# Optimization experiments

Measured on AMD Instinct MI355X. Metric: run time of the kernel, lower is better.

Reference implementation:

```python
import jax, jax.numpy as jnp
import numpy as np

N_NODES = 100000
N_EDGES = 3200000
N_GRAPHS = 64
F_IN = 64
NUM_CLASSES = 10
CHROM = 21


def _glorot(key, shape):
    fan_in, fan_out = shape
    lim = (6.0 / (fan_in + fan_out)) ** 0.5
    return jax.random.uniform(key, shape, jnp.float32, -lim, lim)


def setup_inputs() -> dict:
    key = jax.random.key(0)
    ks = jax.random.split(key, 16)
    x = jax.random.normal(ks[0], (N_NODES, F_IN), jnp.float32)
    edge_index = jax.random.randint(ks[1], (2, N_EDGES), 0, N_NODES, jnp.int32)
    batch = jnp.sort(jax.random.randint(ks[2], (N_NODES,), 0, N_GRAPHS, jnp.int32))
    return {
        "x": x,
        "edge_index": edge_index,
        "batch": batch,
        # SAGEConv1: 64 -> 16
        "W1l": _glorot(ks[3], (F_IN, 16)), "b1": jnp.zeros((16,), jnp.float32),
        "W1r": _glorot(ks[4], (F_IN, 16)),
        # SAGEConv2: 16 -> 32
        "W2l": _glorot(ks[5], (16, 32)), "b2": jnp.zeros((32,), jnp.float32),
        "W2r": _glorot(ks[6], (16, 32)),
        # SAGEConv3: 32 -> 21
        "W3l": _glorot(ks[7], (32, CHROM)), "b3": jnp.zeros((CHROM,), jnp.float32),
        "W3r": _glorot(ks[8], (32, CHROM)),
        # classifier: 32 -> num_classes
        "Wc": _glorot(ks[9], (32, NUM_CLASSES)), "bc": jnp.zeros((NUM_CLASSES,), jnp.float32),
    }


def _sage_conv(x, src, dst, Wl, b, Wr):
    # mean aggregation of source features at target nodes (PyG SAGEConv default)
    agg = jax.ops.segment_sum(x[src], dst, num_segments=N_NODES)
    cnt = jax.ops.segment_sum(jnp.ones((src.shape[0],), x.dtype), dst, num_segments=N_NODES)
    mean = agg / jnp.maximum(cnt, 1.0)[:, None]
    return mean @ Wl + b + x @ Wr


def reference(x, edge_index, batch, W1l, b1, W1r, W2l, b2, W2r, W3l, b3, W3r, Wc, bc):
    src, dst = edge_index[0], edge_index[1]
    h = jax.nn.relu(_sage_conv(x, src, dst, W1l, b1, W1r))
    h2 = _sage_conv(h, src, dst, W2l, b2, W2r)          # pooled pre-relu
    color = _sage_conv(jax.nn.relu(h2), src, dst, W3l, b3, W3r)
    # global_mean_pool over graphs
    gsum = jax.ops.segment_sum(h2, batch, num_segments=N_GRAPHS)
    gcnt = jax.ops.segment_sum(jnp.ones((h2.shape[0],), h2.dtype), batch, num_segments=N_GRAPHS)
    pooled = gsum / jnp.maximum(gcnt, 1.0)[:, None]
    # dropout p=0.3 is identity in eval mode
    classif = pooled @ Wc + bc
    return classif, color
```

## Files before the change

### kernel.cpp

```cpp
#include <hip/hip_runtime.h>
#include <hip/hip_fp16.h>
#include <cstdint>
#include <cstddef>

#define N_NODES  100000
#define N_EDGES  3200000
#define N_GRAPHS 64

#define BQBITS   9
#define BQ       512
#define NBUCK    196
#define TILE     4096
#define NBLK     782
#define POOL_SLICES 8
#define PADB     4608

typedef float vf2 __attribute__((ext_vector_type(2)));


__global__ void kp1_hist(const int* __restrict__ dst, int* __restrict__ gh, int ne) {
    __shared__ int h[NBUCK];
    for (int i = threadIdx.x; i < NBUCK; i += 256) h[i] = 0;
    __syncthreads();
    int base = blockIdx.x * TILE;
    for (int i = threadIdx.x; i < TILE; i += 256) {
        int e = base + i;
        if (e < ne) atomicAdd(&h[dst[e] >> BQBITS], 1);
    }
    __syncthreads();
    for (int i = threadIdx.x; i < NBUCK; i += 256) gh[i * NBLK + blockIdx.x] = h[i];
}

__global__ void kp1_scanA(int* __restrict__ gh, int* __restrict__ btotal) {
    int q = blockIdx.x;
    __shared__ int ts[256];
    int v[4];
    int tsum = 0;
#pragma unroll
    for (int u = 0; u < 4; ++u) {
        int idx = threadIdx.x * 4 + u;
        v[u] = (idx < NBLK) ? gh[q * NBLK + idx] : 0;
        tsum += v[u];
    }
    ts[threadIdx.x] = tsum;
    __syncthreads();
    for (int off = 1; off < 256; off <<= 1) {
        int t = (threadIdx.x >= off) ? ts[threadIdx.x - off] : 0;
        __syncthreads();
        ts[threadIdx.x] += t;
        __syncthreads();
    }
    int run = ts[threadIdx.x] - tsum;
#pragma unroll
    for (int u = 0; u < 4; ++u) {
        int idx = threadIdx.x * 4 + u;
        if (idx < NBLK) gh[q * NBLK + idx] = run;
        run += v[u];
    }
    if (threadIdx.x == 255) btotal[q] = ts[255];
}

__global__ void kp1_scanB(const int* __restrict__ btotal, int* __restrict__ bstart) {
    __shared__ int s[256];
    int v = (threadIdx.x < NBUCK) ? btotal[threadIdx.x] : 0;
    s[threadIdx.x] = v;
    __syncthreads();
    for (int off = 1; off < 256; off <<= 1) {
        int t = (threadIdx.x >= off) ? s[threadIdx.x - off] : 0;
        __syncthreads();
        s[threadIdx.x] += t;
        __syncthreads();
    }
    if (threadIdx.x < NBUCK) bstart[threadIdx.x] = s[threadIdx.x] - v;
    if (threadIdx.x == 0) bstart[NBUCK] = N_EDGES;
}

__global__ __launch_bounds__(256) void kp1_scatter(
        const int* __restrict__ src, const int* __restrict__ dst,
        const int* __restrict__ gh, const int* __restrict__ bstart,
        unsigned* __restrict__ tmp, int ne) {
    __shared__ unsigned sed[TILE];
    __shared__ int lcnt[NBUCK];
    __shared__ int lofs[NBUCK + 1];
    __shared__ int fill[NBUCK];
    __shared__ int delta[NBUCK];
    __shared__ int ts[256];
    for (int i = threadIdx.x; i < NBUCK; i += 256) { lcnt[i] = 0; fill[i] = 0; }
    __syncthreads();
    int base = blockIdx.x * TILE;
    int nh = ne - base; if (nh > TILE) nh = TILE;
    int myq[16]; unsigned myw[16];
#pragma unroll
    for (int u = 0; u < 16; ++u) {
        int i = u * 256 + threadIdx.x;
        myq[u] = -1;
        if (i < nh) {
            int d = dst[base + i], s = src[base + i];
            int q = d >> BQBITS;
            myq[u] = q;
            myw[u] = ((unsigned)(d & (BQ - 1)) << 17) | (unsigned)s;
            atomicAdd(&lcnt[q], 1);
        }
    }
    __syncthreads();
    int v = (threadIdx.x < NBUCK) ? lcnt[threadIdx.x] : 0;
    ts[threadIdx.x] = v;
    __syncthreads();
    for (int off = 1; off < 256; off <<= 1) {
        int t = (threadIdx.x >= off) ? ts[threadIdx.x - off] : 0;
        __syncthreads();
        ts[threadIdx.x] += t;
        __syncthreads();
    }
    if (threadIdx.x < NBUCK) {
        int start = ts[threadIdx.x] - v;
        lofs[threadIdx.x] = start;
        delta[threadIdx.x] = bstart[threadIdx.x] + gh[threadIdx.x * NBLK + blockIdx.x] - start;
    }
    if (threadIdx.x == NBUCK - 1) lofs[NBUCK] = ts[threadIdx.x];
    __syncthreads();
#pragma unroll
    for (int u = 0; u < 16; ++u) {
        if (myq[u] >= 0) {
            int r = atomicAdd(&fill[myq[u]], 1);
            sed[lofs[myq[u]] + r] = myw[u];
        }
    }
    __syncthreads();
    for (int p = threadIdx.x; p < nh; p += 256) {
        int lo = 0, hi = NBUCK;
        while (hi - lo > 1) { int mid = (lo + hi) >> 1; if (lofs[mid] <= p) lo = mid; else hi = mid; }
        tmp[p + delta[lo]] = sed[p];
    }
}

__global__ void kp2(const unsigned* __restrict__ tmp, const int* __restrict__ bstart,
                    int* __restrict__ rs, int* __restrict__ deg, int* __restrict__ perm) {
    int q = blockIdx.x;
    int beg = bstart[q], end = bstart[q + 1];
    int m = end - beg;
    int pbase = ((beg + 7) & ~7) + q * PADB;
    __shared__ int cnt[BQ];
    __shared__ int lofs[BQ];
    __shared__ int fill[BQ];
    if (threadIdx.x < BQ) { cnt[threadIdx.x] = 0; fill[threadIdx.x] = 0; }
    __syncthreads();
    for (int p = threadIdx.x; p < m; p += 1024)
        atomicAdd(&cnt[tmp[beg + p] >> 17], 1);
    __syncthreads();
    int pc = 0;
    if (threadIdx.x < BQ) { pc = (cnt[threadIdx.x] + 7) & ~7; lofs[threadIdx.x] = pc; }
    __syncthreads();
    for (int off = 1; off < BQ; off <<= 1) {
        int t = 0;
        if (threadIdx.x < BQ && threadIdx.x >= off) t = lofs[threadIdx.x - off];
        __syncthreads();
        if (threadIdx.x < BQ) lofs[threadIdx.x] += t;
        __syncthreads();
    }
    if (threadIdx.x < BQ) {
        int node = q * BQ + threadIdx.x;
        if (node < N_NODES) {
            int st = lofs[threadIdx.x] - pc;
            rs[node] = pbase + st;
            deg[node] = cnt[threadIdx.x];
            for (int i = cnt[threadIdx.x]; i < pc; ++i)
                perm[pbase + st + i] = N_NODES;
        }
    }
    __syncthreads();
    for (int p = threadIdx.x; p < m; p += 1024) {
        unsigned w = tmp[beg + p];
        int dl = w >> 17;
        int s = w & 0x1FFFF;
        int r = atomicAdd(&fill[dl], 1);
        int st = lofs[dl] - ((cnt[dl] + 7) & ~7);
        perm[pbase + st + r] = s;
    }
}


__device__ __forceinline__ void accq(uint2 v, float* a) {
    vf2 f0 = __builtin_amdgcn_cvt_pk_f32_fp8((int)v.x, false);
    vf2 f1 = __builtin_amdgcn_cvt_pk_f32_fp8((int)v.x, true);
    vf2 f2 = __builtin_amdgcn_cvt_pk_f32_fp8((int)v.y, false);
    vf2 f3 = __builtin_amdgcn_cvt_pk_f32_fp8((int)v.y, true);
    a[0] += f0.x; a[1] += f0.y; a[2] += f1.x; a[3] += f1.y;
    a[4] += f2.x; a[5] += f2.y; a[6] += f3.x; a[7] += f3.y;
}

__device__ __forceinline__ uint2 pack8_fp8(const float* a) {
    int lo = __builtin_amdgcn_cvt_pk_fp8_f32(a[0], a[1], 0, false);
    lo     = __builtin_amdgcn_cvt_pk_fp8_f32(a[2], a[3], lo, true);
    int hi = __builtin_amdgcn_cvt_pk_fp8_f32(a[4], a[5], 0, false);
    hi     = __builtin_amdgcn_cvt_pk_fp8_f32(a[6], a[7], hi, true);
    uint2 o; o.x = (unsigned)lo; o.y = (unsigned)hi; return o;
}


__global__ void k_zero(uint2* __restrict__ y1qz, uint2* __restrict__ hqz,
                       unsigned char* __restrict__ y3qz, float* __restrict__ gsum) {
    int t = threadIdx.x;
    if (t < 2) { y1qz[t] = make_uint2(0, 0); hqz[t] = make_uint2(0, 0); }
    if (t < 24) y3qz[t] = 0;
    for (int i = t; i < N_GRAPHS * 32; i += 256) gsum[i] = 0.f;
}


__global__ void k_t1(const float* __restrict__ x, const float* __restrict__ W1l,
                     const float* __restrict__ W1r, const float* __restrict__ b1,
                     uint2* __restrict__ y1q, float* __restrict__ s1, int n) {
    __shared__ float wl[64 * 16], wr[64 * 16], bb[16];
    for (int i = threadIdx.x; i < 64 * 16; i += blockDim.x) { wl[i] = W1l[i]; wr[i] = W1r[i]; }
    if (threadIdx.x < 16) bb[threadIdx.x] = b1[threadIdx.x];
    __syncthreads();
    int node = blockIdx.x * blockDim.x + threadIdx.x;
    if (node >= n) return;
    const float4* xr = reinterpret_cast<const float4*>(x + (size_t)node * 64);
    float accl[16], accr[16];
#pragma unroll
    for (int j = 0; j < 16; ++j) { accl[j] = 0.f; accr[j] = 0.f; }
#pragma unroll
    for (int q = 0; q < 16; ++q) {
        float4 v = xr[q];
        float xs[4] = {v.x, v.y, v.z, v.w};
#pragma unroll
        for (int u = 0; u < 4; ++u) {
            int k = q * 4 + u;
            float xv = xs[u];
#pragma unroll
            for (int j = 0; j < 16; ++j) {
                accl[j] += xv * wl[k * 16 + j];
                accr[j] += xv * wr[k * 16 + j];
            }
        }
    }
    y1q[(size_t)node * 2 + 0] = pack8_fp8(accl);
    y1q[(size_t)node * 2 + 1] = pack8_fp8(accl + 8);
    float4* s4 = reinterpret_cast<float4*>(s1 + (size_t)node * 16);
#pragma unroll
    for (int q = 0; q < 4; ++q)
        s4[q] = make_float4(accr[q*4+0] + bb[q*4+0], accr[q*4+1] + bb[q*4+1],
                            accr[q*4+2] + bb[q*4+2], accr[q*4+3] + bb[q*4+3]);
}

__global__ void k_t2(const float* __restrict__ mean2, const __half* __restrict__ h,
                     const float* __restrict__ W2l, const float* __restrict__ W2r,
                     const float* __restrict__ b2, float* __restrict__ h2, int n) {
    __shared__ float wl[16 * 32], wr[16 * 32], bb[32];
    for (int i = threadIdx.x; i < 16 * 32; i += blockDim.x) { wl[i] = W2l[i]; wr[i] = W2r[i]; }
    if (threadIdx.x < 32) bb[threadIdx.x] = b2[threadIdx.x];
    __syncthreads();
    int node = blockIdx.x * blockDim.x + threadIdx.x;
    if (node >= n) return;
    float m[16], hh[16];
    const float4* m4 = reinterpret_cast<const float4*>(mean2 + (size_t)node * 16);
#pragma unroll
    for (int q = 0; q < 4; ++q) {
        float4 a = m4[q];
        m[q*4+0]=a.x; m[q*4+1]=a.y; m[q*4+2]=a.z; m[q*4+3]=a.w;
    }
    alignas(16) __half hv[16];
    const uint4* hp = reinterpret_cast<const uint4*>(h + (size_t)node * 16);
    uint4* hvp = reinterpret_cast<uint4*>(hv);
    hvp[0] = hp[0]; hvp[1] = hp[1];
#pragma unroll
    for (int k = 0; k < 16; ++k) hh[k] = __half2float(hv[k]);
    float acc[32];
#pragma unroll
    for (int j = 0; j < 32; ++j) acc[j] = bb[j];
#pragma unroll
    for (int k = 0; k < 16; ++k) {
#pragma unroll
        for (int j = 0; j < 32; ++j)
            acc[j] += m[k] * wl[k * 32 + j] + hh[k] * wr[k * 32 + j];
    }
    float4* o4 = reinterpret_cast<float4*>(h2 + (size_t)node * 32);
#pragma unroll
    for (int q = 0; q < 8; ++q)
        o4[q] = make_float4(acc[q*4+0], acc[q*4+1], acc[q*4+2], acc[q*4+3]);
}

__global__ void k_t3(const float* __restrict__ h2, const float* __restrict__ W3l,
                     const float* __restrict__ W3r, const float* __restrict__ b3,
                     unsigned char* __restrict__ y3q, float* __restrict__ s3, int n) {
    __shared__ float wl[32 * 21], wr[32 * 21], bb[21];
    for (int i = threadIdx.x; i < 32 * 21; i += blockDim.x) { wl[i] = W3l[i]; wr[i] = W3r[i]; }
    if (threadIdx.x < 21) bb[threadIdx.x] = b3[threadIdx.x];
    __syncthreads();
    int node = blockIdx.x * blockDim.x + threadIdx.x;
    if (node >= n) return;
    float z[32];
    const float4* h4 = reinterpret_cast<const float4*>(h2 + (size_t)node * 32);
#pragma unroll
    for (int q = 0; q < 8; ++q) {
        float4 v = h4[q];
        z[q*4+0] = fmaxf(v.x, 0.f); z[q*4+1] = fmaxf(v.y, 0.f);
        z[q*4+2] = fmaxf(v.z, 0.f); z[q*4+3] = fmaxf(v.w, 0.f);
    }
    float a[24], c[21];
#pragma unroll
    for (int j = 0; j < 21; ++j) { a[j] = 0.f; c[j] = bb[j]; }
    a[21] = 0.f; a[22] = 0.f; a[23] = 0.f;
#pragma unroll
    for (int k = 0; k < 32; ++k) {
#pragma unroll
        for (int j = 0; j < 21; ++j) {
            a[j] += z[k] * wl[k * 21 + j];
            c[j] += z[k] * wr[k * 21 + j];
        }
    }
    uint2* yp = reinterpret_cast<uint2*>(y3q + (size_t)node * 24);
    yp[0] = pack8_fp8(a);
    yp[1] = pack8_fp8(a + 8);
    yp[2] = pack8_fp8(a + 16);
    float* so = s3 + (size_t)node * 24;
#pragma unroll
    for (int j = 0; j < 21; ++j) so[j] = c[j];
    so[21] = 0.f; so[22] = 0.f; so[23] = 0.f;
}


__global__ void k_agg_l1(const uint2* __restrict__ yq, const int* __restrict__ rs,
                         const int* __restrict__ deg, const int* __restrict__ perm,
                         const float* __restrict__ s1, __half* __restrict__ h,
                         uint2* __restrict__ hq, int n_nodes) {
    int t = blockIdx.x * blockDim.x + threadIdx.x;
    int node = t >> 1;
    int f = t & 1;
    if (node >= n_nodes) return;
    int beg = rs[node];
    int d = deg[node];
    int pend = beg + ((d + 7) & ~7);
    float a[8];
#pragma unroll
    for (int j = 0; j < 8; ++j) a[j] = 0.f;
    for (int e = beg; e < pend; e += 8) {
        const int4* pp = reinterpret_cast<const int4*>(perm + e);
        int4 p0 = pp[0];
        int4 p1 = pp[1];
        uint2 v0 = yq[(size_t)p0.x * 2 + f];
        uint2 v1 = yq[(size_t)p0.y * 2 + f];
        uint2 v2 = yq[(size_t)p0.z * 2 + f];
        uint2 v3 = yq[(size_t)p0.w * 2 + f];
        uint2 v4 = yq[(size_t)p1.x * 2 + f];
        uint2 v5 = yq[(size_t)p1.y * 2 + f];
        uint2 v6 = yq[(size_t)p1.z * 2 + f];
        uint2 v7 = yq[(size_t)p1.w * 2 + f];
        accq(v0, a); accq(v1, a); accq(v2, a); accq(v3, a);
        accq(v4, a); accq(v5, a); accq(v6, a); accq(v7, a);
    }
    float inv = 1.0f / fmaxf((float)d, 1.0f);
    const float4* sp = reinterpret_cast<const float4*>(s1 + (size_t)node * 16 + f * 8);
    float4 s0 = sp[0], s1v = sp[1];
    a[0] = fmaxf(a[0] * inv + s0.x, 0.f);
    a[1] = fmaxf(a[1] * inv + s0.y, 0.f);
    a[2] = fmaxf(a[2] * inv + s0.z, 0.f);
    a[3] = fmaxf(a[3] * inv + s0.w, 0.f);
    a[4] = fmaxf(a[4] * inv + s1v.x, 0.f);
    a[5] = fmaxf(a[5] * inv + s1v.y, 0.f);
    a[6] = fmaxf(a[6] * inv + s1v.z, 0.f);
    a[7] = fmaxf(a[7] * inv + s1v.w, 0.f);
    __half2 p0h = __floats2half2_rn(a[0], a[1]);
    __half2 p1h = __floats2half2_rn(a[2], a[3]);
    __half2 p2h = __floats2half2_rn(a[4], a[5]);
    __half2 p3h = __floats2half2_rn(a[6], a[7]);
    uint4 o;
    o.x = *reinterpret_cast<unsigned*>(&p0h);
    o.y = *reinterpret_cast<unsigned*>(&p1h);
    o.z = *reinterpret_cast<unsigned*>(&p2h);
    o.w = *reinterpret_cast<unsigned*>(&p3h);
    reinterpret_cast<uint4*>(h)[(size_t)node * 2 + f] = o;
    hq[(size_t)node * 2 + f] = pack8_fp8(a);
}

__global__ void k_agg_l2(const uint2* __restrict__ hq, const int* __restrict__ rs,
                         const int* __restrict__ deg, const int* __restrict__ perm,
                         float* __restrict__ mean2, int n_nodes) {
    int t = blockIdx.x * blockDim.x + threadIdx.x;
    int node = t >> 1;
    int f = t & 1;
    if (node >= n_nodes) return;
    int beg = rs[node];
    int d = deg[node];
    int pend = beg + ((d + 7) & ~7);
    float a[8];
#pragma unroll
    for (int j = 0; j < 8; ++j) a[j] = 0.f;
    for (int e = beg; e < pend; e += 8) {
        const int4* pp = reinterpret_cast<const int4*>(perm + e);
        int4 p0 = pp[0];
        int4 p1 = pp[1];
        uint2 v0 = hq[(size_t)p0.x * 2 + f];
        uint2 v1 = hq[(size_t)p0.y * 2 + f];
        uint2 v2 = hq[(size_t)p0.z * 2 + f];
        uint2 v3 = hq[(size_t)p0.w * 2 + f];
        uint2 v4 = hq[(size_t)p1.x * 2 + f];
        uint2 v5 = hq[(size_t)p1.y * 2 + f];
        uint2 v6 = hq[(size_t)p1.z * 2 + f];
        uint2 v7 = hq[(size_t)p1.w * 2 + f];
        accq(v0, a); accq(v1, a); accq(v2, a); accq(v3, a);
        accq(v4, a); accq(v5, a); accq(v6, a); accq(v7, a);
    }
    float inv = 1.0f / fmaxf((float)d, 1.0f);
    float4* op = reinterpret_cast<float4*>(mean2 + (size_t)node * 16 + f * 8);
    op[0] = make_float4(a[0] * inv, a[1] * inv, a[2] * inv, a[3] * inv);
    op[1] = make_float4(a[4] * inv, a[5] * inv, a[6] * inv, a[7] * inv);
}

__global__ void k_agg_l3(const unsigned char* __restrict__ y3q, const int* __restrict__ rs,
                         const int* __restrict__ deg, const int* __restrict__ perm,
                         const float* __restrict__ self24, float* __restrict__ outp,
                         int n_nodes) {
    int t = blockIdx.x * blockDim.x + threadIdx.x;
    int node = t / 3;
    int f = t - node * 3;
    if (node >= n_nodes) return;
    const uint2* yq = reinterpret_cast<const uint2*>(y3q);
    int beg = rs[node];
    int d = deg[node];
    int pend = beg + ((d + 7) & ~7);
    float a[8];
#pragma unroll
    for (int j = 0; j < 8; ++j) a[j] = 0.f;
    for (int e = beg; e < pend; e += 8) {
        const int4* pp = reinterpret_cast<const int4*>(perm + e);
        int4 p0 = pp[0];
        int4 p1 = pp[1];
        uint2 v0 = yq[(size_t)p0.x * 3 + f];
        uint2 v1 = yq[(size_t)p0.y * 3 + f];
        uint2 v2 = yq[(size_t)p0.z * 3 + f];
        uint2 v3 = yq[(size_t)p0.w * 3 + f];
        uint2 v4 = yq[(size_t)p1.x * 3 + f];
        uint2 v5 = yq[(size_t)p1.y * 3 + f];
        uint2 v6 = yq[(size_t)p1.z * 3 + f];
        uint2 v7 = yq[(size_t)p1.w * 3 + f];
        accq(v0, a); accq(v1, a); accq(v2, a); accq(v3, a);
        accq(v4, a); accq(v5, a); accq(v6, a); accq(v7, a);
    }
    float inv = 1.0f / fmaxf((float)d, 1.0f);
    int c0 = f * 8;
    const float4* sp = reinterpret_cast<const float4*>(self24 + (size_t)node * 24 + c0);
    float4 s0 = sp[0], s1 = sp[1];
    float r[8];
    r[0] = a[0] * inv + s0.x; r[1] = a[1] * inv + s0.y;
    r[2] = a[2] * inv + s0.z; r[3] = a[3] * inv + s0.w;
    r[4] = a[4] * inv + s1.x; r[5] = a[5] * inv + s1.y;
    r[6] = a[6] * inv + s1.z; r[7] = a[7] * inv + s1.w;
    float* op = outp + (size_t)node * 21;
    int nlim = 21 - c0;
#pragma unroll
    for (int j = 0; j < 8; ++j)
        if (j < nlim) op[c0 + j] = r[j];
}


__device__ __forceinline__ int lowerb(const int* a, int n, int key) {
    int lo = 0, hi = n;
    while (lo < hi) { int mid = (lo + hi) >> 1; if (a[mid] < key) lo = mid + 1; else hi = mid; }
    return lo;
}

__global__ void k_pool(const float* __restrict__ h2, const int* __restrict__ batch,
                       float* __restrict__ gsum, float* __restrict__ gcnt, int n) {
    int g = blockIdx.x / POOL_SLICES;
    int slice = blockIdx.x - g * POOL_SLICES;
    __shared__ int sbeg, send;
    if (threadIdx.x == 0) { sbeg = lowerb(batch, n, g); send = lowerb(batch, n, g + 1); }
    __syncthreads();
    int beg = sbeg, end = send;
    int f = threadIdx.x & 31;
    int r = threadIdx.x >> 5;
    float acc = 0.f;
    for (int i = beg + slice * 8 + r; i < end; i += POOL_SLICES * 8)
        acc += h2[(size_t)i * 32 + f];
    __shared__ float red[256];
    red[threadIdx.x] = acc;
    __syncthreads();
    if (r == 0) {
        float s = 0.f;
#pragma unroll
        for (int q = 0; q < 8; ++q) s += red[q * 32 + f];
        atomicAdd(&gsum[g * 32 + f], s);
    }
    if (slice == 0 && threadIdx.x == 0) gcnt[g] = (float)(end - beg);
}

__global__ void k_cls(const float* __restrict__ gsum, const float* __restrict__ gcnt,
                      const float* __restrict__ Wc, const float* __restrict__ bc,
                      float* __restrict__ outp) {
    int t = threadIdx.x;
    if (t >= N_GRAPHS * 10) return;
    int g = t / 10, c = t - g * 10;
    float cv = fmaxf(gcnt[g], 1.f);
    float acc = bc[c];
#pragma unroll
    for (int k = 0; k < 32; ++k) acc += (gsum[g * 32 + k] / cv) * Wc[k * 10 + c];
    outp[g * 10 + c] = acc;
}


extern "C" void kernel_launch(void* const* d_in, const int* in_sizes, int n_in,
                              void* d_out, int out_size, void* d_ws, size_t ws_size,
                              hipStream_t stream) {
    const float* x    = (const float*)d_in[0];
    const int*   ei   = (const int*)d_in[1];
    const int*   batch= (const int*)d_in[2];
    const float* W1l  = (const float*)d_in[3];
    const float* b1   = (const float*)d_in[4];
    const float* W1r  = (const float*)d_in[5];
    const float* W2l  = (const float*)d_in[6];
    const float* b2   = (const float*)d_in[7];
    const float* W2r  = (const float*)d_in[8];
    const float* W3l  = (const float*)d_in[9];
    const float* b3   = (const float*)d_in[10];
    const float* W3r  = (const float*)d_in[11];
    const float* Wc   = (const float*)d_in[12];
    const float* bc   = (const float*)d_in[13];
    float* out = (float*)d_out;

    char* ws = (char*)d_ws;
    size_t off = 0;
    auto alloc = [&](size_t bytes) { size_t o = off; off += (bytes + 255) & ~(size_t)255; return o; };

    int*    rs    = (int*)(ws + alloc((size_t)N_NODES * 4));
    int*    deg   = (int*)(ws + alloc((size_t)N_NODES * 4));
    int*    perm  = (int*)(ws + alloc((size_t)(N_EDGES + (size_t)NBUCK * PADB + 64) * 4));
    int*    gh    = (int*)(ws + alloc((size_t)NBUCK * NBLK * 4));
    int*    btotal= (int*)(ws + alloc(256 * 4));
    int*    bstart= (int*)(ws + alloc(260 * 4));
    uint2*  y1q   = (uint2*)(ws + alloc((size_t)(N_NODES + 1) * 16));
    float*  s1    = (float*)(ws + alloc((size_t)N_NODES * 16 * 4));
    __half* h     = (__half*)(ws + alloc((size_t)N_NODES * 16 * 2));
    uint2*  hq    = (uint2*)(ws + alloc((size_t)(N_NODES + 1) * 16));
    float*  mean2 = (float*)(ws + alloc((size_t)N_NODES * 16 * 4));
    float*  h2    = (float*)(ws + alloc((size_t)N_NODES * 32 * 4));
    unsigned char* y3q = (unsigned char*)(ws + alloc((size_t)(N_NODES + 1) * 24));
    float*  s3    = (float*)(ws + alloc((size_t)N_NODES * 24 * 4));
    float*  gsum  = (float*)(ws + alloc((size_t)N_GRAPHS * 32 * 4));
    float*  gcnt  = (float*)(ws + alloc((size_t)N_GRAPHS * 4));

    unsigned* tmp = (unsigned*)h2;

    const int* src = ei;
    const int* dst = ei + N_EDGES;

    int nb  = (N_NODES + 255) / 256;
    int g2  = (N_NODES * 2 + 255) / 256;
    int g3  = (N_NODES * 3 + 255) / 256;

    k_zero<<<1, 256, 0, stream>>>(y1q + (size_t)N_NODES * 2, hq + (size_t)N_NODES * 2,
                                  y3q + (size_t)N_NODES * 24, gsum);

    kp1_hist   <<<NBLK, 256, 0, stream>>>(dst, gh, N_EDGES);
    kp1_scanA  <<<NBUCK, 256, 0, stream>>>(gh, btotal);
    kp1_scanB  <<<1, 256, 0, stream>>>(btotal, bstart);
    kp1_scatter<<<NBLK, 256, 0, stream>>>(src, dst, gh, bstart, tmp, N_EDGES);
    kp2        <<<NBUCK, 1024, 0, stream>>>(tmp, bstart, rs, deg, perm);

    k_t1<<<nb, 256, 0, stream>>>(x, W1l, W1r, b1, y1q, s1, N_NODES);
    k_agg_l1<<<g2, 256, 0, stream>>>(y1q, rs, deg, perm, s1, h, hq, N_NODES);

    k_agg_l2<<<g2, 256, 0, stream>>>(hq, rs, deg, perm, mean2, N_NODES);
    k_t2<<<nb, 256, 0, stream>>>(mean2, h, W2l, W2r, b2, h2, N_NODES);

    k_t3<<<nb, 256, 0, stream>>>(h2, W3l, W3r, b3, y3q, s3, N_NODES);
    k_agg_l3<<<g3, 256, 0, stream>>>(y3q, rs, deg, perm, s3, out + N_GRAPHS * 10, N_NODES);

    k_pool<<<N_GRAPHS * POOL_SLICES, 256, 0, stream>>>(h2, batch, gsum, gcnt, N_NODES);
    k_cls<<<1, 640, 0, stream>>>(gsum, gcnt, Wc, bc, out);
}
```

Before: 214.9 us.

## Fuse layer-2/3 transforms with graph pooling and drop zero kernel

Merges the k_t2 and k_t3 node transforms into one kernel, so h2 stays in registers and is no longer written to and re-read from global memory. Each block reduces its h2 rows per graph in shared memory and atomically adds them into gsum, which replaces the separate pooling kernel. The zeroing work moves into scanB, and graph counts are now computed by binary search inside k_cls, together removing three launches. The cost is a large shared buffer that may reduce occupancy, a serial 256-row reduction done by a single wavefront per block, and tmp now needing its own workspace allocation.

Measured after the change: 203.0 us. 5.5% less time.

```diff
diff --git a/kernel.cpp b/kernel.cpp
--- a/kernel.cpp
+++ b/kernel.cpp
@@ -12,7 +12,6 @@
 #define NBUCK    196
 #define TILE     4096
 #define NBLK     782
-#define POOL_SLICES 8
 #define PADB     4608
 
 typedef float vf2 __attribute__((ext_vector_type(2)));
@@ -60,7 +59,9 @@
     if (threadIdx.x == 255) btotal[q] = ts[255];
 }
 
-__global__ void kp1_scanB(const int* __restrict__ btotal, int* __restrict__ bstart) {
+__global__ void kp1_scanB(const int* __restrict__ btotal, int* __restrict__ bstart,
+                          uint2* __restrict__ y1qz, uint2* __restrict__ hqz,
+                          unsigned char* __restrict__ y3qz, float* __restrict__ gsum) {
     __shared__ int s[256];
     int v = (threadIdx.x < NBUCK) ? btotal[threadIdx.x] : 0;
     s[threadIdx.x] = v;
@@ -73,6 +74,10 @@
     }
     if (threadIdx.x < NBUCK) bstart[threadIdx.x] = s[threadIdx.x] - v;
     if (threadIdx.x == 0) bstart[NBUCK] = N_EDGES;
+    int t = threadIdx.x;
+    if (t < 2) { y1qz[t] = make_uint2(0, 0); hqz[t] = make_uint2(0, 0); }
+    if (t < 24) y3qz[t] = 0;
+    for (int i = t; i < N_GRAPHS * 32; i += 256) gsum[i] = 0.f;
 }
 
 __global__ __launch_bounds__(256) void kp1_scatter(
@@ -198,15 +203,6 @@
 }
 
 
-__global__ void k_zero(uint2* __restrict__ y1qz, uint2* __restrict__ hqz,
-                       unsigned char* __restrict__ y3qz, float* __restrict__ gsum) {
-    int t = threadIdx.x;
-    if (t < 2) { y1qz[t] = make_uint2(0, 0); hqz[t] = make_uint2(0, 0); }
-    if (t < 24) y3qz[t] = 0;
-    for (int i = t; i < N_GRAPHS * 32; i += 256) gsum[i] = 0.f;
-}
-
-
 __global__ void k_t1(const float* __restrict__ x, const float* __restrict__ W1l,
                      const float* __restrict__ W1r, const float* __restrict__ b1,
                      uint2* __restrict__ y1q, float* __restrict__ s1, int n) {
@@ -244,80 +240,94 @@
                             accr[q*4+2] + bb[q*4+2], accr[q*4+3] + bb[q*4+3]);
 }
 
-__global__ void k_t2(const float* __restrict__ mean2, const __half* __restrict__ h,
-                     const float* __restrict__ W2l, const float* __restrict__ W2r,
-                     const float* __restrict__ b2, float* __restrict__ h2, int n) {
-    __shared__ float wl[16 * 32], wr[16 * 32], bb[32];
-    for (int i = threadIdx.x; i < 16 * 32; i += blockDim.x) { wl[i] = W2l[i]; wr[i] = W2r[i]; }
-    if (threadIdx.x < 32) bb[threadIdx.x] = b2[threadIdx.x];
-    __syncthreads();
-    int node = blockIdx.x * blockDim.x + threadIdx.x;
-    if (node >= n) return;
+__global__ __launch_bounds__(256) void k_t23(
+        const float* __restrict__ mean2, const __half* __restrict__ h,
+        const float* __restrict__ W2l, const float* __restrict__ W2r,
+        const float* __restrict__ b2,
+        const float* __restrict__ W3l, const float* __restrict__ W3r,
+        const float* __restrict__ b3,
+        const int* __restrict__ batch,
+        unsigned char* __restrict__ y3q, float* __restrict__ s3,
+        float* __restrict__ gsum, int n) {
+    __shared__ float wl2[16 * 32], wr2[16 * 32], bb2[32];
+    __shared__ float wl3[32 * 21], wr3[32 * 21], bb3[21];
+    __shared__ float buf[256][33];
+    __shared__ int sbatch[256];
+    for (int i = threadIdx.x; i < 16 * 32; i += 256) { wl2[i] = W2l[i]; wr2[i] = W2r[i]; }
+    for (int i = threadIdx.x; i < 32 * 21; i += 256) { wl3[i] = W3l[i]; wr3[i] = W3r[i]; }
+    if (threadIdx.x < 32) bb2[threadIdx.x] = b2[threadIdx.x];
+    if (threadIdx.x < 21) bb3[threadIdx.x] = b3[threadIdx.x];
+    __syncthreads();
+    int node = blockIdx.x * 256 + threadIdx.x;
+    bool valid = node < n;
+    int nodeC = valid ? node : (n - 1);
+
     float m[16], hh[16];
-    const float4* m4 = reinterpret_cast<const float4*>(mean2 + (size_t)node * 16);
-#pragma unroll
-    for (int q = 0; q < 4; ++q) {
-        float4 a = m4[q];
-        m[q*4+0]=a.x; m[q*4+1]=a.y; m[q*4+2]=a.z; m[q*4+3]=a.w;
-    }
-    alignas(16) __half hv[16];
-    const uint4* hp = reinterpret_cast<const uint4*>(h + (size_t)node * 16);
-    uint4* hvp = reinterpret_cast<uint4*>(hv);
-    hvp[0] = hp[0]; hvp[1] = hp[1];
-#pragma unroll
-    for (int k = 0; k < 16; ++k) hh[k] = __half2float(hv[k]);
+    {
+        const float4* m4 = reinterpret_cast<const float4*>(mean2 + (size_t)nodeC * 16);
+#pragma unroll
+        for (int q = 0; q < 4; ++q) {
+            float4 a = m4[q];
+            m[q*4+0]=a.x; m[q*4+1]=a.y; m[q*4+2]=a.z; m[q*4+3]=a.w;
+        }
+        alignas(16) __half hv[16];
+        const uint4* hp = reinterpret_cast<const uint4*>(h + (size_t)nodeC * 16);
+        reinterpret_cast<uint4*>(hv)[0] = hp[0];
+        reinterpret_cast<uint4*>(hv)[1] = hp[1];
+#pragma unroll
+        for (int k = 0; k < 16; ++k) hh[k] = __half2float(hv[k]);
+    }
     float acc[32];
 #pragma unroll
-    for (int j = 0; j < 32; ++j) acc[j] = bb[j];
+    for (int j = 0; j < 32; ++j) acc[j] = bb2[j];
 #pragma unroll
     for (int k = 0; k < 16; ++k) {
 #pragma unroll
         for (int j = 0; j < 32; ++j)
-            acc[j] += m[k] * wl[k * 32 + j] + hh[k] * wr[k * 32 + j];
-    }
-    float4* o4 = reinterpret_cast<float4*>(h2 + (size_t)node * 32);
-#pragma unroll
-    for (int q = 0; q < 8; ++q)
-        o4[q] = make_float4(acc[q*4+0], acc[q*4+1], acc[q*4+2], acc[q*4+3]);
-}
-
-__global__ void k_t3(const float* __restrict__ h2, const float* __restrict__ W3l,
-                     const float* __restrict__ W3r, const float* __restrict__ b3,
-                     unsigned char* __restrict__ y3q, float* __restrict__ s3, int n) {
-    __shared__ float wl[32 * 21], wr[32 * 21], bb[21];
-    for (int i = threadIdx.x; i < 32 * 21; i += blockDim.x) { wl[i] = W3l[i]; wr[i] = W3r[i]; }
-    if (threadIdx.x < 21) bb[threadIdx.x] = b3[threadIdx.x];
-    __syncthreads();
-    int node = blockIdx.x * blockDim.x + threadIdx.x;
-    if (node >= n) return;
+            acc[j] += m[k] * wl2[k * 32 + j] + hh[k] * wr2[k * 32 + j];
+    }
+#pragma unroll
+    for (int j = 0; j < 32; ++j) buf[threadIdx.x][j] = valid ? acc[j] : 0.f;
+    sbatch[threadIdx.x] = batch[nodeC];
+    __syncthreads();
+
     float z[32];
-    const float4* h4 = reinterpret_cast<const float4*>(h2 + (size_t)node * 32);
-#pragma unroll
-    for (int q = 0; q < 8; ++q) {
-        float4 v = h4[q];
-        z[q*4+0] = fmaxf(v.x, 0.f); z[q*4+1] = fmaxf(v.y, 0.f);
-        z[q*4+2] = fmaxf(v.z, 0.f); z[q*4+3] = fmaxf(v.w, 0.f);
-    }
+#pragma unroll
+    for (int j = 0; j < 32; ++j) z[j] = fmaxf(acc[j], 0.f);
     float a[24], c[21];
 #pragma unroll
-    for (int j = 0; j < 21; ++j) { a[j] = 0.f; c[j] = bb[j]; }
+    for (int j = 0; j < 21; ++j) { a[j] = 0.f; c[j] = bb3[j]; }
     a[21] = 0.f; a[22] = 0.f; a[23] = 0.f;
 #pragma unroll
     for (int k = 0; k < 32; ++k) {
 #pragma unroll
         for (int j = 0; j < 21; ++j) {
-            a[j] += z[k] * wl[k * 21 + j];
-            c[j] += z[k] * wr[k * 21 + j];
-        }
-    }
-    uint2* yp = reinterpret_cast<uint2*>(y3q + (size_t)node * 24);
-    yp[0] = pack8_fp8(a);
-    yp[1] = pack8_fp8(a + 8);
-    yp[2] = pack8_fp8(a + 16);
-    float* so = s3 + (size_t)node * 24;
-#pragma unroll
-    for (int j = 0; j < 21; ++j) so[j] = c[j];
-    so[21] = 0.f; so[22] = 0.f; so[23] = 0.f;
+            a[j] += z[k] * wl3[k * 21 + j];
+            c[j] += z[k] * wr3[k * 21 + j];
+        }
+    }
+    if (valid) {
+        uint2* yp = reinterpret_cast<uint2*>(y3q + (size_t)node * 24);
+        yp[0] = pack8_fp8(a);
+        yp[1] = pack8_fp8(a + 8);
+        yp[2] = pack8_fp8(a + 16);
+        float* so = s3 + (size_t)node * 24;
+#pragma unroll
+        for (int j = 0; j < 21; ++j) so[j] = c[j];
+        so[21] = 0.f; so[22] = 0.f; so[23] = 0.f;
+    }
+
+    if (threadIdx.x < 32) {
+        int f = threadIdx.x;
+        int cur = sbatch[0];
+        float s = 0.f;
+        for (int r = 0; r < 256; ++r) {
+            int g = sbatch[r];
+            if (g != cur) { atomicAdd(&gsum[cur * 32 + f], s); s = 0.f; cur = g; }
+            s += buf[r][f];
+        }
+        atomicAdd(&gsum[cur * 32 + f], s);
+    }
 }
 
 
@@ -461,38 +471,15 @@
     return lo;
 }
 
-__global__ void k_pool(const float* __restrict__ h2, const int* __restrict__ batch,
-                       float* __restrict__ gsum, float* __restrict__ gcnt, int n) {
-    int g = blockIdx.x / POOL_SLICES;
-    int slice = blockIdx.x - g * POOL_SLICES;
-    __shared__ int sbeg, send;
-    if (threadIdx.x == 0) { sbeg = lowerb(batch, n, g); send = lowerb(batch, n, g + 1); }
-    __syncthreads();
-    int beg = sbeg, end = send;
-    int f = threadIdx.x & 31;
-    int r = threadIdx.x >> 5;
-    float acc = 0.f;
-    for (int i = beg + slice * 8 + r; i < end; i += POOL_SLICES * 8)
-        acc += h2[(size_t)i * 32 + f];
-    __shared__ float red[256];
-    red[threadIdx.x] = acc;
-    __syncthreads();
-    if (r == 0) {
-        float s = 0.f;
-#pragma unroll
-        for (int q = 0; q < 8; ++q) s += red[q * 32 + f];
-        atomicAdd(&gsum[g * 32 + f], s);
-    }
-    if (slice == 0 && threadIdx.x == 0) gcnt[g] = (float)(end - beg);
-}
-
-__global__ void k_cls(const float* __restrict__ gsum, const float* __restrict__ gcnt,
+__global__ void k_cls(const float* __restrict__ gsum, const int* __restrict__ batch,
                       const float* __restrict__ Wc, const float* __restrict__ bc,
                       float* __restrict__ outp) {
     int t = threadIdx.x;
     if (t >= N_GRAPHS * 10) return;
     int g = t / 10, c = t - g * 10;
-    float cv = fmaxf(gcnt[g], 1.f);
+    int beg = lowerb(batch, N_NODES, g);
+    int end = lowerb(batch, N_NODES, g + 1);
+    float cv = fmaxf((float)(end - beg), 1.f);
     float acc = bc[c];
 #pragma unroll
     for (int k = 0; k < 32; ++k) acc += (gsum[g * 32 + k] / cv) * Wc[k * 10 + c];
@@ -529,18 +516,15 @@
     int*    gh    = (int*)(ws + alloc((size_t)NBUCK * NBLK * 4));
     int*    btotal= (int*)(ws + alloc(256 * 4));
     int*    bstart= (int*)(ws + alloc(260 * 4));
+    unsigned* tmp = (unsigned*)(ws + alloc((size_t)N_EDGES * 4));
     uint2*  y1q   = (uint2*)(ws + alloc((size_t)(N_NODES + 1) * 16));
     float*  s1    = (float*)(ws + alloc((size_t)N_NODES * 16 * 4));
     __half* h     = (__half*)(ws + alloc((size_t)N_NODES * 16 * 2));
     uint2*  hq    = (uint2*)(ws + alloc((size_t)(N_NODES + 1) * 16));
     float*  mean2 = (float*)(ws + alloc((size_t)N_NODES * 16 * 4));
-    float*  h2    = (float*)(ws + alloc((size_t)N_NODES * 32 * 4));
     unsigned char* y3q = (unsigned char*)(ws + alloc((size_t)(N_NODES + 1) * 24));
     float*  s3    = (float*)(ws + alloc((size_t)N_NODES * 24 * 4));
     float*  gsum  = (float*)(ws + alloc((size_t)N_GRAPHS * 32 * 4));
-    float*  gcnt  = (float*)(ws + alloc((size_t)N_GRAPHS * 4));
-
-    unsigned* tmp = (unsigned*)h2;
 
     const int* src = ei;
     const int* dst = ei + N_EDGES;
@@ -549,12 +533,11 @@
     int g2  = (N_NODES * 2 + 255) / 256;
     int g3  = (N_NODES * 3 + 255) / 256;
 
-    k_zero<<<1, 256, 0, stream>>>(y1q + (size_t)N_NODES * 2, hq + (size_t)N_NODES * 2,
-                                  y3q + (size_t)N_NODES * 24, gsum);
-
     kp1_hist   <<<NBLK, 256, 0, stream>>>(dst, gh, N_EDGES);
     kp1_scanA  <<<NBUCK, 256, 0, stream>>>(gh, btotal);
-    kp1_scanB  <<<1, 256, 0, stream>>>(btotal, bstart);
+    kp1_scanB  <<<1, 256, 0, stream>>>(btotal, bstart,
+                                       y1q + (size_t)N_NODES * 2, hq + (size_t)N_NODES * 2,
+                                       y3q + (size_t)N_NODES * 24, gsum);
     kp1_scatter<<<NBLK, 256, 0, stream>>>(src, dst, gh, bstart, tmp, N_EDGES);
     kp2        <<<NBUCK, 1024, 0, stream>>>(tmp, bstart, rs, deg, perm);
 
@@ -562,11 +545,11 @@
     k_agg_l1<<<g2, 256, 0, stream>>>(y1q, rs, deg, perm, s1, h, hq, N_NODES);
 
     k_agg_l2<<<g2, 256, 0, stream>>>(hq, rs, deg, perm, mean2, N_NODES);
-    k_t2<<<nb, 256, 0, stream>>>(mean2, h, W2l, W2r, b2, h2, N_NODES);
-
-    k_t3<<<nb, 256, 0, stream>>>(h2, W3l, W3r, b3, y3q, s3, N_NODES);
+
+    k_t23<<<nb, 256, 0, stream>>>(mean2, h, W2l, W2r, b2, W3l, W3r, b3,
+                                  batch, y3q, s3, gsum, N_NODES);
+
     k_agg_l3<<<g3, 256, 0, stream>>>(y3q, rs, deg, perm, s3, out + N_GRAPHS * 10, N_NODES);
 
-    k_pool<<<N_GRAPHS * POOL_SLICES, 256, 0, stream>>>(h2, batch, gsum, gcnt, N_NODES);
-    k_cls<<<1, 640, 0, stream>>>(gsum, gcnt, Wc, bc, out);
-}
+    k_cls<<<1, 640, 0, stream>>>(gsum, batch, Wc, bc, out);
+}
```
